# Performance work log

Measured on AMD Instinct MI355X. Metric: run time of the kernel, lower is better.

## Reference

```python
import jax, jax.numpy as jnp
import numpy as np

NEG_SLOPE = 0.2  # GATConv attention leaky_relu slope (init arg)
POST_SLOPE = 0.2  # leaky_relu after LayerNorm in outer forward
N_LAYERS = 3


def _leaky(x, slope):
    return jnp.where(x >= 0, x, slope * x)


def _layer_norm(x, g, b):
    mu = jnp.mean(x, axis=-1, keepdims=True)
    var = jnp.var(x, axis=-1, keepdims=True)
    return (x - mu) * jax.lax.rsqrt(var + 1e-5) * g + b


def _gat_conv(h, W, al, ar, bias, src, dst, apply_act):
    # DGL GATConv (eval mode, dropout = identity)
    N = h.shape[0]
    H, D = al.shape
    feat = (h @ W).reshape(N, H, D)                      # [N,H,D]
    el = jnp.einsum('nhd,hd->nh', feat, al)              # [N,H]
    er = jnp.einsum('nhd,hd->nh', feat, ar)              # [N,H]
    e = _leaky(el[src] + er[dst], NEG_SLOPE)             # [E,H] edge logits
    # segment (per-destination) softmax, numerically stable
    m = jax.ops.segment_max(e, dst, num_segments=N)      # [N,H]
    ex = jnp.exp(e - m[dst])                             # [E,H]
    s = jax.ops.segment_sum(ex, dst, num_segments=N)     # [N,H]
    alpha = ex / s[dst]                                  # [E,H]
    msg = alpha[:, :, None] * feat[src]                  # [E,H,D]
    rst = jax.ops.segment_sum(msg, dst, num_segments=N)  # [N,H,D]
    rst = rst + bias.reshape(1, H, D)
    if apply_act:
        rst = jax.nn.elu(rst)
    return rst


def setup_inputs() -> dict:
    key = jax.random.key(0)
    ks = jax.random.split(key, 12)
    N, E, IN, D, H, C = 100000, 1600000, 256, 64, 4, 40
    HID = H * D  # 256
    sc = 0.05
    return {
        'x': jax.random.normal(ks[0], (N, IN), jnp.float32),
        'W_h': jax.random.normal(ks[1], (3, IN, HID), jnp.float32) * sc,
        'attn_l_h': jax.random.normal(ks[2], (3, H, D), jnp.float32) * sc,
        'attn_r_h': jax.random.normal(ks[3], (3, H, D), jnp.float32) * sc,
        'bias_h': jnp.zeros((3, HID), jnp.float32),
        'ln_g': jnp.ones((3, HID), jnp.float32),
        'ln_b': jnp.zeros((3, HID), jnp.float32),
        'W_o': jax.random.normal(ks[4], (HID, C), jnp.float32) * sc,
        'attn_l_o': jax.random.normal(ks[5], (1, C), jnp.float32) * sc,
        'attn_r_o': jax.random.normal(ks[6], (1, C), jnp.float32) * sc,
        'bias_o': jnp.zeros((C,), jnp.float32),
        'edge_src': jax.random.randint(ks[7], (E,), 0, N, jnp.int32),
        'edge_dst': jax.random.randint(ks[8], (E,), 0, N, jnp.int32),
    }


def reference(x, W_h, attn_l_h, attn_r_h, bias_h, ln_g, ln_b,
              W_o, attn_l_o, attn_r_o, bias_o, edge_src, edge_dst):
    h = x
    for l in range(N_LAYERS):
        hn = _gat_conv(h, W_h[l], attn_l_h[l], attn_r_h[l], bias_h[l],
                       edge_src, edge_dst, True)
        hn = hn.reshape(hn.shape[0], -1)          # flatten heads -> [N, H*D]
        hn = _layer_norm(hn, ln_g[l], ln_b[l])
        hn = _leaky(hn, POST_SLOPE)
        h = hn + h if h.shape == hn.shape else hn  # residual when shapes match
    logits = _gat_conv(h, W_o, attn_l_o, attn_r_o, bias_o,
                       edge_src, edge_dst, False).sum(axis=1)  # sum over heads
    return logits
```

## Files before the change

kernel.cpp:

```cpp
#include <hip/hip_runtime.h>
#include <math.h>


#define NEG_SLOPE 0.2f

typedef __attribute__((ext_vector_type(8))) short bf16x8;
typedef __attribute__((ext_vector_type(4))) float floatx4;

__device__ __forceinline__ float leaky(float x) { return x >= 0.f ? x : NEG_SLOPE * x; }

__device__ __forceinline__ unsigned short f2bf(float f) {
    unsigned u = __builtin_bit_cast(unsigned, f);
    u += 0x7fffu + ((u >> 16) & 1u);
    return (unsigned short)(u >> 16);
}
__device__ __forceinline__ float bf2f(unsigned short h) {
    unsigned u = ((unsigned)h) << 16;
    return __builtin_bit_cast(float, u);
}

typedef const __attribute__((address_space(1))) unsigned int* as1_u32p;
typedef __attribute__((address_space(3))) unsigned int* as3_u32p;
__device__ __forceinline__ void gl_lds16(const void* g, void* l) {
    __builtin_amdgcn_global_load_lds((as1_u32p)g, (as3_u32p)l, 16, 0, 0);
}

__global__ void zero_i32(int* __restrict__ p, int n) {
    int i = blockIdx.x * blockDim.x + threadIdx.x;
    if (i < n) p[i] = 0;
}

__global__ void hist_kernel(const int* __restrict__ dst, int* __restrict__ counts, int E) {
    int e = blockIdx.x * blockDim.x + threadIdx.x;
    if (e < E) atomicAdd(&counts[dst[e]], 1);
}

__global__ void alloc_kernel(const int* __restrict__ counts, int* __restrict__ start,
                             int* __restrict__ cursor, int* __restrict__ total, int N) {
    int n = blockIdx.x * blockDim.x + threadIdx.x;
    if (n < N) {
        int c = counts[n];
        int s = atomicAdd(total, c);
        start[n] = s;
        cursor[n] = s;
    }
}

__global__ void scatter_kernel(const int* __restrict__ src, const int* __restrict__ dst,
                               int* __restrict__ cursor, int* __restrict__ col, int E) {
    int e = blockIdx.x * blockDim.x + threadIdx.x;
    if (e < E) {
        int p = atomicAdd(&cursor[dst[e]], 1);
        col[p] = src[e];
    }
}

__global__ void convert_bf(const float* __restrict__ src, unsigned short* __restrict__ dst,
                           int n4) {
    int i = blockIdx.x * blockDim.x + threadIdx.x;
    if (i < n4) {
        float4 v = *(const float4*)(src + (size_t)i * 4);
        ushort4 s;
        s.x = f2bf(v.x); s.y = f2bf(v.y); s.z = f2bf(v.z); s.w = f2bf(v.w);
        *(ushort4*)(dst + (size_t)i * 4) = s;
    }
}

__global__ void transpose_w(const float* __restrict__ W, unsigned short* __restrict__ Wt) {
    int idx = blockIdx.x * 256 + threadIdx.x;
    int l = idx >> 16, r = idx & 65535;
    int k = r >> 8, n = r & 255;
    Wt[l * 65536 + n * 256 + k] = f2bf(W[l * 65536 + k * 256 + n]);
}

__global__ void transpose_wo(const float* __restrict__ W, unsigned short* __restrict__ Wt) {
    int idx = blockIdx.x * 256 + threadIdx.x;
    int n = idx >> 8, k = idx & 255;
    Wt[n * 256 + k] = (n < 40) ? f2bf(W[k * 40 + n]) : (unsigned short)0;
}

__global__ __launch_bounds__(512, 4) void gemm_bf16_fused(
    const unsigned short* __restrict__ A, const unsigned short* __restrict__ Wt,
    const float* __restrict__ al, const float* __restrict__ ar,
    unsigned short* __restrict__ Cb, float* __restrict__ el, float* __restrict__ er, int M) {
    __shared__ unsigned short As[2][128 * 32];
    __shared__ unsigned short Bs[2][256 * 32];
    const int tid = threadIdx.x;
    const int row0 = blockIdx.x * 128;
    const int lane = tid & 63, wid = tid >> 6;
    const int wm = (wid >> 2) * 64;
    const int wn = (wid & 3) * 64;

    const int arow = wid * 16 + (lane >> 2);
    const int brow0 = wid * 32 + (lane >> 2);
    const int kx = (lane & 3) * 8;
    const int agr = (row0 + arow < M) ? (row0 + arow) : (M - 1);

    auto stage = [&](int buf, int kb) {
        gl_lds16(A + (size_t)agr * 256 + kb + kx, &As[buf][arow * 32 + kx]);
        gl_lds16(Wt + (size_t)brow0 * 256 + kb + kx, &Bs[buf][brow0 * 32 + kx]);
        gl_lds16(Wt + (size_t)(brow0 + 16) * 256 + kb + kx, &Bs[buf][(brow0 + 16) * 32 + kx]);
    };

    floatx4 acc[4][4] = {};
    const int q = lane >> 4, m = lane & 15;

    stage(0, 0);
    __syncthreads();
    int cur = 0;
    for (int kb = 0; kb < 256; kb += 32) {
        int nkb = kb + 32;
        if (nkb < 256) stage(cur ^ 1, nkb);
        bf16x8 af[4], bfr[4];
#pragma unroll
        for (int i = 0; i < 4; ++i) {
            af[i] = *(const bf16x8*)&As[cur][(wm + i * 16 + m) * 32 + q * 8];
            bfr[i] = *(const bf16x8*)&Bs[cur][(wn + i * 16 + m) * 32 + q * 8];
        }
#pragma unroll
        for (int i = 0; i < 4; ++i)
#pragma unroll
            for (int j = 0; j < 4; ++j)
                acc[i][j] = __builtin_amdgcn_mfma_f32_16x16x32_bf16(af[i], bfr[j], acc[i][j], 0, 0, 0);
        __syncthreads();
        cur ^= 1;
    }

    const int c = lane & 15;
#pragma unroll
    for (int i = 0; i < 4; ++i)
#pragma unroll
        for (int j = 0; j < 4; ++j)
#pragma unroll
            for (int r = 0; r < 4; ++r) {
                int grow = row0 + wm + i * 16 + q * 4 + r;
                int gcol = wn + j * 16 + c;
                if (grow < M) Cb[(size_t)grow * 256 + gcol] = f2bf(acc[i][j][r]);
            }

    const int head = wid & 3;
    const float* alh = al + head * 64;
    const float* arh = ar + head * 64;
    float a0 = alh[c], a1 = alh[16 + c], a2 = alh[32 + c], a3 = alh[48 + c];
    float r0 = arh[c], r1 = arh[16 + c], r2 = arh[32 + c], r3 = arh[48 + c];
#pragma unroll
    for (int i = 0; i < 4; ++i)
#pragma unroll
        for (int r = 0; r < 4; ++r) {
            float pel = acc[i][0][r] * a0 + acc[i][1][r] * a1 + acc[i][2][r] * a2 + acc[i][3][r] * a3;
            float per = acc[i][0][r] * r0 + acc[i][1][r] * r1 + acc[i][2][r] * r2 + acc[i][3][r] * r3;
#pragma unroll
            for (int off = 8; off >= 1; off >>= 1) {
                pel += __shfl_xor(pel, off);
                per += __shfl_xor(per, off);
            }
            if (c == 0) {
                int grow = row0 + wm + i * 16 + q * 4 + r;
                if (grow < M) {
                    el[(size_t)grow * 4 + head] = pel;
                    er[(size_t)grow * 4 + head] = per;
                }
            }
        }
}

#define LDSK 40
#define BSTRIDE 264
__global__ __launch_bounds__(256) void gemm_out_mfma(const unsigned short* __restrict__ h,
                                                     const unsigned short* __restrict__ Wt,
                                                     const float* __restrict__ alo,
                                                     const float* __restrict__ aro,
                                                     unsigned short* __restrict__ feat_o,
                                                     float* __restrict__ elo,
                                                     float* __restrict__ ero, int N) {
    __shared__ unsigned short As[128 * LDSK];
    __shared__ unsigned short Bs[48 * BSTRIDE];
    const int tid = threadIdx.x;
    const int row0 = blockIdx.x * 128;
    const int lane = tid & 63, wid = tid >> 6;

#pragma unroll
    for (int i = 0; i < 6; ++i) {
        int f = tid + 256 * i;
        int n = f >> 5, kk = (f & 31) * 8;
        *(bf16x8*)&Bs[n * BSTRIDE + kk] = *(const bf16x8*)(Wt + n * 256 + kk);
    }
    __syncthreads();

    floatx4 acc[2][3] = {};
    for (int kb = 0; kb < 256; kb += 32) {
#pragma unroll
        for (int i = 0; i < 2; ++i) {
            int idx = tid + 256 * i;
            int r = idx >> 2, k8 = (idx & 3) * 8;
            int gr = row0 + r;
            bf16x8 v = {};
            if (gr < N) v = *(const bf16x8*)(h + (size_t)gr * 256 + kb + k8);
            *(bf16x8*)&As[r * LDSK + k8] = v;
        }
        __syncthreads();
        const int q = lane >> 4, m = lane & 15;
        bf16x8 af[2], bfr[3];
#pragma unroll
        for (int i = 0; i < 2; ++i)
            af[i] = *(const bf16x8*)&As[(wid * 32 + i * 16 + m) * LDSK + q * 8];
#pragma unroll
        for (int j = 0; j < 3; ++j)
            bfr[j] = *(const bf16x8*)&Bs[(j * 16 + m) * BSTRIDE + kb + q * 8];
#pragma unroll
        for (int i = 0; i < 2; ++i)
#pragma unroll
            for (int j = 0; j < 3; ++j)
                acc[i][j] = __builtin_amdgcn_mfma_f32_16x16x32_bf16(af[i], bfr[j], acc[i][j], 0, 0, 0);
        __syncthreads();
    }

    const int q = lane >> 4, c = lane & 15;
#pragma unroll
    for (int i = 0; i < 2; ++i)
#pragma unroll
        for (int j = 0; j < 3; ++j)
#pragma unroll
            for (int r = 0; r < 4; ++r) {
                int grow = row0 + wid * 32 + i * 16 + q * 4 + r;
                int gcol = j * 16 + c;
                if (grow < N && gcol < 40) feat_o[(size_t)grow * 40 + gcol] = f2bf(acc[i][j][r]);
            }

    float aj[3], rj[3];
#pragma unroll
    for (int j = 0; j < 3; ++j) {
        int gcol = j * 16 + c;
        aj[j] = gcol < 40 ? alo[gcol] : 0.f;
        rj[j] = gcol < 40 ? aro[gcol] : 0.f;
    }
#pragma unroll
    for (int i = 0; i < 2; ++i)
#pragma unroll
        for (int r = 0; r < 4; ++r) {
            float pl = acc[i][0][r] * aj[0] + acc[i][1][r] * aj[1] + acc[i][2][r] * aj[2];
            float pr = acc[i][0][r] * rj[0] + acc[i][1][r] * rj[1] + acc[i][2][r] * rj[2];
#pragma unroll
            for (int off = 8; off >= 1; off >>= 1) {
                pl += __shfl_xor(pl, off);
                pr += __shfl_xor(pr, off);
            }
            if (c == 0) {
                int grow = row0 + wid * 32 + i * 16 + q * 4 + r;
                if (grow < N) {
                    elo[grow] = pl;
                    ero[grow] = pr;
                }
            }
        }
}

__global__ __launch_bounds__(256) void aggregate_hidden(
    const unsigned short* __restrict__ feat, const float* __restrict__ el,
    const float* __restrict__ er, const int* __restrict__ start, const int* __restrict__ endp,
    const int* __restrict__ col, const float* __restrict__ bias, const float* __restrict__ lng,
    const float* __restrict__ lnb, const unsigned short* __restrict__ h_in,
    unsigned short* __restrict__ h_out, int N) {
    int node = blockIdx.x * 4 + (threadIdx.x >> 6);
    int lane = threadIdx.x & 63;
    if (node >= N) return;
    int begin = __builtin_amdgcn_readfirstlane(start[node]);
    int end = __builtin_amdgcn_readfirstlane(endp[node]);
    const int head = lane >> 4;
    const float erh = er[(size_t)node * 4 + head];

    const int ch = lane * 4;
    const unsigned short* fbase = feat + ch;
    const size_t hstr = 256;
    float4 acc = {0.f, 0.f, 0.f, 0.f};
    float ssum = 0.f;
    int e = begin;
    for (; e + 7 < end; e += 8) {
        int sA = col[e], sB = col[e + 1], sC = col[e + 2], sD = col[e + 3];
        int sE = col[e + 4], sF = col[e + 5], sG = col[e + 6], sH = col[e + 7];
        float eA = el[(size_t)sA * 4 + head];
        float eB = el[(size_t)sB * 4 + head];
        float eC = el[(size_t)sC * 4 + head];
        float eD = el[(size_t)sD * 4 + head];
        float eE = el[(size_t)sE * 4 + head];
        float eF = el[(size_t)sF * 4 + head];
        float eG = el[(size_t)sG * 4 + head];
        float eH = el[(size_t)sH * 4 + head];
        ushort4 uA = *(const ushort4*)(fbase + sA * hstr);
        ushort4 uB = *(const ushort4*)(fbase + sB * hstr);
        ushort4 uC = *(const ushort4*)(fbase + sC * hstr);
        ushort4 uD = *(const ushort4*)(fbase + sD * hstr);
        ushort4 uE = *(const ushort4*)(fbase + sE * hstr);
        ushort4 uF = *(const ushort4*)(fbase + sF * hstr);
        ushort4 uG = *(const ushort4*)(fbase + sG * hstr);
        ushort4 uH = *(const ushort4*)(fbase + sH * hstr);
        float wA = __expf(leaky(eA + erh));
        float wB = __expf(leaky(eB + erh));
        float wC = __expf(leaky(eC + erh));
        float wD = __expf(leaky(eD + erh));
        float wE = __expf(leaky(eE + erh));
        float wF = __expf(leaky(eF + erh));
        float wG = __expf(leaky(eG + erh));
        float wH = __expf(leaky(eH + erh));
        ssum += wA + wB + wC + wD + wE + wF + wG + wH;
        acc.x = fmaf(wA, bf2f(uA.x), acc.x); acc.y = fmaf(wA, bf2f(uA.y), acc.y);
        acc.z = fmaf(wA, bf2f(uA.z), acc.z); acc.w = fmaf(wA, bf2f(uA.w), acc.w);
        acc.x = fmaf(wB, bf2f(uB.x), acc.x); acc.y = fmaf(wB, bf2f(uB.y), acc.y);
        acc.z = fmaf(wB, bf2f(uB.z), acc.z); acc.w = fmaf(wB, bf2f(uB.w), acc.w);
        acc.x = fmaf(wC, bf2f(uC.x), acc.x); acc.y = fmaf(wC, bf2f(uC.y), acc.y);
        acc.z = fmaf(wC, bf2f(uC.z), acc.z); acc.w = fmaf(wC, bf2f(uC.w), acc.w);
        acc.x = fmaf(wD, bf2f(uD.x), acc.x); acc.y = fmaf(wD, bf2f(uD.y), acc.y);
        acc.z = fmaf(wD, bf2f(uD.z), acc.z); acc.w = fmaf(wD, bf2f(uD.w), acc.w);
        acc.x = fmaf(wE, bf2f(uE.x), acc.x); acc.y = fmaf(wE, bf2f(uE.y), acc.y);
        acc.z = fmaf(wE, bf2f(uE.z), acc.z); acc.w = fmaf(wE, bf2f(uE.w), acc.w);
        acc.x = fmaf(wF, bf2f(uF.x), acc.x); acc.y = fmaf(wF, bf2f(uF.y), acc.y);
        acc.z = fmaf(wF, bf2f(uF.z), acc.z); acc.w = fmaf(wF, bf2f(uF.w), acc.w);
        acc.x = fmaf(wG, bf2f(uG.x), acc.x); acc.y = fmaf(wG, bf2f(uG.y), acc.y);
        acc.z = fmaf(wG, bf2f(uG.z), acc.z); acc.w = fmaf(wG, bf2f(uG.w), acc.w);
        acc.x = fmaf(wH, bf2f(uH.x), acc.x); acc.y = fmaf(wH, bf2f(uH.y), acc.y);
        acc.z = fmaf(wH, bf2f(uH.z), acc.z); acc.w = fmaf(wH, bf2f(uH.w), acc.w);
    }
    for (; e < end; ++e) {
        int sA = col[e];
        float wA = __expf(leaky(el[(size_t)sA * 4 + head] + erh));
        ushort4 uA = *(const ushort4*)(fbase + sA * hstr);
        ssum += wA;
        acc.x = fmaf(wA, bf2f(uA.x), acc.x); acc.y = fmaf(wA, bf2f(uA.y), acc.y);
        acc.z = fmaf(wA, bf2f(uA.z), acc.z); acc.w = fmaf(wA, bf2f(uA.w), acc.w);
    }
    float inv = ssum > 0.f ? 1.f / ssum : 0.f;
    acc.x *= inv; acc.y *= inv; acc.z *= inv; acc.w *= inv;

    float4 bb = *(const float4*)(bias + ch);
    float x0 = acc.x + bb.x, x1 = acc.y + bb.y, x2 = acc.z + bb.z, x3 = acc.w + bb.w;
    x0 = x0 > 0.f ? x0 : expm1f(x0);
    x1 = x1 > 0.f ? x1 : expm1f(x1);
    x2 = x2 > 0.f ? x2 : expm1f(x2);
    x3 = x3 > 0.f ? x3 : expm1f(x3);
    float lsum = x0 + x1 + x2 + x3;
    float lsq = x0 * x0 + x1 * x1 + x2 * x2 + x3 * x3;
#pragma unroll
    for (int off = 32; off >= 1; off >>= 1) {
        lsum += __shfl_xor(lsum, off);
        lsq += __shfl_xor(lsq, off);
    }
    float mu = lsum * (1.f / 256.f);
    float var = lsq * (1.f / 256.f) - mu * mu;
    float rstd = rsqrtf(var + 1e-5f);
    float4 g4 = *(const float4*)(lng + ch);
    float4 b4 = *(const float4*)(lnb + ch);
    ushort4 hi = *(const ushort4*)(h_in + (size_t)node * 256 + ch);
    float y0 = (x0 - mu) * rstd * g4.x + b4.x;
    float y1 = (x1 - mu) * rstd * g4.y + b4.y;
    float y2 = (x2 - mu) * rstd * g4.z + b4.z;
    float y3 = (x3 - mu) * rstd * g4.w + b4.w;
    y0 = (y0 >= 0.f ? y0 : 0.2f * y0) + bf2f(hi.x);
    y1 = (y1 >= 0.f ? y1 : 0.2f * y1) + bf2f(hi.y);
    y2 = (y2 >= 0.f ? y2 : 0.2f * y2) + bf2f(hi.z);
    y3 = (y3 >= 0.f ? y3 : 0.2f * y3) + bf2f(hi.w);
    ushort4 o;
    o.x = f2bf(y0); o.y = f2bf(y1); o.z = f2bf(y2); o.w = f2bf(y3);
    *(ushort4*)(h_out + (size_t)node * 256 + ch) = o;
}

__global__ __launch_bounds__(256) void aggregate_out(const unsigned short* __restrict__ feat_o,
                                                     const float* __restrict__ elo,
                                                     const float* __restrict__ ero,
                                                     const int* __restrict__ start,
                                                     const int* __restrict__ endp,
                                                     const int* __restrict__ col,
                                                     const float* __restrict__ bias_o,
                                                     float* __restrict__ out, int N) {
    int node = blockIdx.x * 4 + (threadIdx.x >> 6);
    int lane = threadIdx.x & 63;
    if (node >= N) return;
    int begin = __builtin_amdgcn_readfirstlane(start[node]);
    int end = __builtin_amdgcn_readfirstlane(endp[node]);
    float ern = ero[node];
    int cc = lane < 40 ? lane : 0;
    float acc = 0.f, ssum = 0.f;
    int e = begin;
    for (; e + 7 < end; e += 8) {
        int sA = col[e], sB = col[e + 1], sC = col[e + 2], sD = col[e + 3];
        int sE = col[e + 4], sF = col[e + 5], sG = col[e + 6], sH = col[e + 7];
        float eA = elo[sA], eB = elo[sB], eC = elo[sC], eD = elo[sD];
        float eE = elo[sE], eF = elo[sF], eG = elo[sG], eH = elo[sH];
        unsigned short fA = feat_o[(size_t)sA * 40 + cc];
        unsigned short fB = feat_o[(size_t)sB * 40 + cc];
        unsigned short fC = feat_o[(size_t)sC * 40 + cc];
        unsigned short fD = feat_o[(size_t)sD * 40 + cc];
        unsigned short fE = feat_o[(size_t)sE * 40 + cc];
        unsigned short fF = feat_o[(size_t)sF * 40 + cc];
        unsigned short fG = feat_o[(size_t)sG * 40 + cc];
        unsigned short fH = feat_o[(size_t)sH * 40 + cc];
        float wA = __expf(leaky(eA + ern));
        float wB = __expf(leaky(eB + ern));
        float wC = __expf(leaky(eC + ern));
        float wD = __expf(leaky(eD + ern));
        float wE = __expf(leaky(eE + ern));
        float wF = __expf(leaky(eF + ern));
        float wG = __expf(leaky(eG + ern));
        float wH = __expf(leaky(eH + ern));
        ssum += wA + wB + wC + wD + wE + wF + wG + wH;
        acc = fmaf(wA, bf2f(fA), acc);
        acc = fmaf(wB, bf2f(fB), acc);
        acc = fmaf(wC, bf2f(fC), acc);
        acc = fmaf(wD, bf2f(fD), acc);
        acc = fmaf(wE, bf2f(fE), acc);
        acc = fmaf(wF, bf2f(fF), acc);
        acc = fmaf(wG, bf2f(fG), acc);
        acc = fmaf(wH, bf2f(fH), acc);
    }
    for (; e < end; ++e) {
        int sA = col[e];
        float wA = __expf(leaky(elo[sA] + ern));
        ssum += wA;
        acc = fmaf(wA, bf2f(feat_o[(size_t)sA * 40 + cc]), acc);
    }
    float inv = ssum > 0.f ? 1.f / ssum : 0.f;
    if (lane < 40) out[(size_t)node * 40 + lane] = acc * inv + bias_o[lane];
}

extern "C" void kernel_launch(void* const* d_in, const int* in_sizes, int n_in,
                              void* d_out, int out_size, void* d_ws, size_t ws_size,
                              hipStream_t stream) {
    const float* x = (const float*)d_in[0];
    const float* W_h = (const float*)d_in[1];
    const float* al_h = (const float*)d_in[2];
    const float* ar_h = (const float*)d_in[3];
    const float* bias_h = (const float*)d_in[4];
    const float* ln_g = (const float*)d_in[5];
    const float* ln_b = (const float*)d_in[6];
    const float* W_o = (const float*)d_in[7];
    const float* al_o = (const float*)d_in[8];
    const float* ar_o = (const float*)d_in[9];
    const float* bias_o = (const float*)d_in[10];
    const int* esrc = (const int*)d_in[11];
    const int* edst = (const int*)d_in[12];
    const int N = in_sizes[0] / 256;
    const int E = in_sizes[11];
    float* out = (float*)d_out;

    char* ws = (char*)d_ws;
    size_t off = 0;
    auto walloc = [&](size_t bytes) -> void* {
        void* p = ws + off;
        off += (bytes + 255) & ~(size_t)255;
        return p;
    };
    unsigned short* x_bf = (unsigned short*)walloc((size_t)N * 256 * 2);
    unsigned short* h_bf = (unsigned short*)walloc((size_t)N * 256 * 2);
    unsigned short* feat_bf = (unsigned short*)walloc((size_t)N * 256 * 2);
    unsigned short* Wt = (unsigned short*)walloc((size_t)3 * 65536 * 2);
    unsigned short* Wt_o = (unsigned short*)walloc((size_t)48 * 256 * 2);
    float* el = (float*)walloc((size_t)N * 4 * 4);
    float* er = (float*)walloc((size_t)N * 4 * 4);
    int* counts = (int*)walloc(((size_t)N + 1) * 4);
    int* start = (int*)walloc((size_t)N * 4);
    int* endp = (int*)walloc((size_t)N * 4);
    int* col = (int*)walloc((size_t)E * 4);
    if (off > ws_size) return;

    const int TB = 256;
    convert_bf<<<(N * 64 + TB - 1) / TB, TB, 0, stream>>>(x, x_bf, N * 64);
    transpose_w<<<3 * 65536 / TB, TB, 0, stream>>>(W_h, Wt);
    transpose_wo<<<48, TB, 0, stream>>>(W_o, Wt_o);
    zero_i32<<<(N + 1 + TB - 1) / TB, TB, 0, stream>>>(counts, N + 1);
    hist_kernel<<<(E + TB - 1) / TB, TB, 0, stream>>>(edst, counts, E);
    alloc_kernel<<<(N + TB - 1) / TB, TB, 0, stream>>>(counts, start, endp, counts + N, N);
    scatter_kernel<<<(E + TB - 1) / TB, TB, 0, stream>>>(esrc, edst, endp, col, E);

    const int nb4 = (N + 3) / 4;
    const int gemm_grid = (N + 127) / 128;
    for (int l = 0; l < 3; ++l) {
        const unsigned short* hin = (l == 0) ? x_bf : h_bf;
        gemm_bf16_fused<<<gemm_grid, 512, 0, stream>>>(hin, Wt + (size_t)l * 65536,
                                                       al_h + l * 256, ar_h + l * 256,
                                                       feat_bf, el, er, N);
        aggregate_hidden<<<nb4, 256, 0, stream>>>(feat_bf, el, er, start, endp, col,
                                                  bias_h + l * 256, ln_g + l * 256,
                                                  ln_b + l * 256, hin, h_bf, N);
    }
    unsigned short* feat_o = feat_bf;
    float* elo = el;
    float* ero = er;
    gemm_out_mfma<<<(N + 127) / 128, 256, 0, stream>>>(h_bf, Wt_o, al_o, ar_o, feat_o, elo, ero, N);
    aggregate_out<<<nb4, 256, 0, stream>>>(feat_o, elo, ero, start, endp, col, bias_o, out, N);
}
```

Measured before the change: 986.9 us.

## Make hidden GEMM persistent with full weight matrix resident in LDS

The hidden-layer GEMM now launches a fixed grid of 256 blocks that loop over 128-row tiles. Each block loads the whole 256x256 bf16 weight matrix into padded LDS once, instead of restaging weight slices on every k-step of every tile. A tiles are now register-prefetched and stored into padded, double-buffered LDS rather than loaded with direct global-to-LDS copies. This cuts repeated weight traffic and launch overhead, but the much larger LDS footprint reduces occupancy (launch bounds lowered to 2) and limits latency hiding.

```diff
diff --git a/kernel.cpp b/kernel.cpp
--- a/kernel.cpp
+++ b/kernel.cpp
@@ -17,12 +17,6 @@
 __device__ __forceinline__ float bf2f(unsigned short h) {
     unsigned u = ((unsigned)h) << 16;
     return __builtin_bit_cast(float, u);
-}
-
-typedef const __attribute__((address_space(1))) unsigned int* as1_u32p;
-typedef __attribute__((address_space(3))) unsigned int* as3_u32p;
-__device__ __forceinline__ void gl_lds16(const void* g, void* l) {
-    __builtin_amdgcn_global_load_lds((as1_u32p)g, (as3_u32p)l, 16, 0, 0);
 }
 
 __global__ void zero_i32(int* __restrict__ p, int n) {
@@ -79,89 +73,95 @@
     Wt[n * 256 + k] = (n < 40) ? f2bf(W[k * 40 + n]) : (unsigned short)0;
 }
 
-__global__ __launch_bounds__(512, 4) void gemm_bf16_fused(
+#define BPAD 264
+#define ALD 40
+__global__ __launch_bounds__(512, 2) void gemm_bf16_fused(
     const unsigned short* __restrict__ A, const unsigned short* __restrict__ Wt,
     const float* __restrict__ al, const float* __restrict__ ar,
     unsigned short* __restrict__ Cb, float* __restrict__ el, float* __restrict__ er, int M) {
-    __shared__ unsigned short As[2][128 * 32];
-    __shared__ unsigned short Bs[2][256 * 32];
+    __shared__ unsigned short Bs[256 * BPAD];
+    __shared__ unsigned short As[2][128 * ALD];
     const int tid = threadIdx.x;
-    const int row0 = blockIdx.x * 128;
     const int lane = tid & 63, wid = tid >> 6;
     const int wm = (wid >> 2) * 64;
     const int wn = (wid & 3) * 64;
-
-    const int arow = wid * 16 + (lane >> 2);
-    const int brow0 = wid * 32 + (lane >> 2);
-    const int kx = (lane & 3) * 8;
-    const int agr = (row0 + arow < M) ? (row0 + arow) : (M - 1);
-
-    auto stage = [&](int buf, int kb) {
-        gl_lds16(A + (size_t)agr * 256 + kb + kx, &As[buf][arow * 32 + kx]);
-        gl_lds16(Wt + (size_t)brow0 * 256 + kb + kx, &Bs[buf][brow0 * 32 + kx]);
-        gl_lds16(Wt + (size_t)(brow0 + 16) * 256 + kb + kx, &Bs[buf][(brow0 + 16) * 32 + kx]);
-    };
-
-    floatx4 acc[4][4] = {};
     const int q = lane >> 4, m = lane & 15;
 
-    stage(0, 0);
+#pragma unroll
+    for (int i = 0; i < 16; ++i) {
+        int flat = tid + 512 * i;
+        int row = flat >> 5, col8 = (flat & 31) * 8;
+        *(bf16x8*)&Bs[row * BPAD + col8] = *(const bf16x8*)(Wt + row * 256 + col8);
+    }
     __syncthreads();
-    int cur = 0;
-    for (int kb = 0; kb < 256; kb += 32) {
-        int nkb = kb + 32;
-        if (nkb < 256) stage(cur ^ 1, nkb);
-        bf16x8 af[4], bfr[4];
-#pragma unroll
-        for (int i = 0; i < 4; ++i) {
-            af[i] = *(const bf16x8*)&As[cur][(wm + i * 16 + m) * 32 + q * 8];
-            bfr[i] = *(const bf16x8*)&Bs[cur][(wn + i * 16 + m) * 32 + q * 8];
-        }
-#pragma unroll
-        for (int i = 0; i < 4; ++i)
-#pragma unroll
-            for (int j = 0; j < 4; ++j)
-                acc[i][j] = __builtin_amdgcn_mfma_f32_16x16x32_bf16(af[i], bfr[j], acc[i][j], 0, 0, 0);
-        __syncthreads();
-        cur ^= 1;
-    }
-
-    const int c = lane & 15;
-#pragma unroll
-    for (int i = 0; i < 4; ++i)
-#pragma unroll
-        for (int j = 0; j < 4; ++j)
-#pragma unroll
-            for (int r = 0; r < 4; ++r) {
-                int grow = row0 + wm + i * 16 + q * 4 + r;
-                int gcol = wn + j * 16 + c;
-                if (grow < M) Cb[(size_t)grow * 256 + gcol] = f2bf(acc[i][j][r]);
-            }
-
+
+    const int rA = tid >> 2, k8 = (tid & 3) * 8;
     const int head = wid & 3;
     const float* alh = al + head * 64;
     const float* arh = ar + head * 64;
+    const int c = lane & 15;
     float a0 = alh[c], a1 = alh[16 + c], a2 = alh[32 + c], a3 = alh[48 + c];
     float r0 = arh[c], r1 = arh[16 + c], r2 = arh[32 + c], r3 = arh[48 + c];
-#pragma unroll
-    for (int i = 0; i < 4; ++i)
-#pragma unroll
-        for (int r = 0; r < 4; ++r) {
-            float pel = acc[i][0][r] * a0 + acc[i][1][r] * a1 + acc[i][2][r] * a2 + acc[i][3][r] * a3;
-            float per = acc[i][0][r] * r0 + acc[i][1][r] * r1 + acc[i][2][r] * r2 + acc[i][3][r] * r3;
-#pragma unroll
-            for (int off = 8; off >= 1; off >>= 1) {
-                pel += __shfl_xor(pel, off);
-                per += __shfl_xor(per, off);
+
+    const int ntiles = (M + 127) >> 7;
+    for (int t = blockIdx.x; t < ntiles; t += gridDim.x) {
+        const int row0 = t << 7;
+        int agr = row0 + rA; if (agr >= M) agr = M - 1;
+        const unsigned short* arow = A + (size_t)agr * 256 + k8;
+        bf16x8 pa = *(const bf16x8*)arow;
+
+        floatx4 acc[4][4] = {};
+        int cur = 0;
+        for (int kb = 0; kb < 256; kb += 32) {
+            *(bf16x8*)&As[cur][rA * ALD + k8] = pa;
+            __syncthreads();
+            if (kb + 32 < 256) pa = *(const bf16x8*)(arow + kb + 32);
+            bf16x8 af[4], bfr[4];
+#pragma unroll
+            for (int i = 0; i < 4; ++i) {
+                af[i] = *(const bf16x8*)&As[cur][(wm + i * 16 + m) * ALD + q * 8];
+                bfr[i] = *(const bf16x8*)&Bs[(wn + i * 16 + m) * BPAD + kb + q * 8];
             }
-            if (c == 0) {
-                int grow = row0 + wm + i * 16 + q * 4 + r;
-                if (grow < M) {
-                    el[(size_t)grow * 4 + head] = pel;
-                    er[(size_t)grow * 4 + head] = per;
+#pragma unroll
+            for (int i = 0; i < 4; ++i)
+#pragma unroll
+                for (int j = 0; j < 4; ++j)
+                    acc[i][j] = __builtin_amdgcn_mfma_f32_16x16x32_bf16(af[i], bfr[j], acc[i][j], 0, 0, 0);
+            cur ^= 1;
+        }
+
+#pragma unroll
+        for (int i = 0; i < 4; ++i)
+#pragma unroll
+            for (int j = 0; j < 4; ++j)
+#pragma unroll
+                for (int r = 0; r < 4; ++r) {
+                    int grow = row0 + wm + i * 16 + q * 4 + r;
+                    int gcol = wn + j * 16 + c;
+                    if (grow < M) Cb[(size_t)grow * 256 + gcol] = f2bf(acc[i][j][r]);
+                }
+
+#pragma unroll
+        for (int i = 0; i < 4; ++i)
+#pragma unroll
+            for (int r = 0; r < 4; ++r) {
+                float pel = acc[i][0][r] * a0 + acc[i][1][r] * a1 + acc[i][2][r] * a2 + acc[i][3][r] * a3;
+                float per = acc[i][0][r] * r0 + acc[i][1][r] * r1 + acc[i][2][r] * r2 + acc[i][3][r] * r3;
+#pragma unroll
+                for (int off = 8; off >= 1; off >>= 1) {
+                    pel += __shfl_xor(pel, off);
+                    per += __shfl_xor(per, off);
+                }
+                if (c == 0) {
+                    int grow = row0 + wm + i * 16 + q * 4 + r;
+                    if (grow < M) {
+                        el[(size_t)grow * 4 + head] = pel;
+                        er[(size_t)grow * 4 + head] = per;
+                    }
                 }
             }
-        }
+        __syncthreads();
+    }
 }
 
 #define LDSK 40
@@ -471,12 +471,11 @@
     scatter_kernel<<<(E + TB - 1) / TB, TB, 0, stream>>>(esrc, edst, endp, col, E);
 
     const int nb4 = (N + 3) / 4;
-    const int gemm_grid = (N + 127) / 128;
     for (int l = 0; l < 3; ++l) {
         const unsigned short* hin = (l == 0) ? x_bf : h_bf;
-        gemm_bf16_fused<<<gemm_grid, 512, 0, stream>>>(hin, Wt + (size_t)l * 65536,
-                                                       al_h + l * 256, ar_h + l * 256,
-                                                       feat_bf, el, er, N);
+        gemm_bf16_fused<<<256, 512, 0, stream>>>(hin, Wt + (size_t)l * 65536,
+                                                 al_h + l * 256, ar_h + l * 256,
+                                                 feat_bf, el, er, N);
         aggregate_hidden<<<nb4, 256, 0, stream>>>(feat_bf, el, er, start, endp, col,
                                                   bias_h + l * 256, ln_g + l * 256,
                                                   ln_b + l * 256, hin, h_bf, N);
```

Result: no change. 992.1 us (+0.5%).
